# Performance work log

Measured on AMD Instinct MI355X. Metric: run time of the kernel, lower is better.

## Reference

```python
import jax, jax.numpy as jnp
import numpy as np

D_MODEL = 1024
NUM_HEADS = 16
HEAD_DIM = D_MODEL // NUM_HEADS
SCALE = HEAD_DIM ** -0.5


def setup_inputs() -> dict:
    key = jax.random.key(0)
    k1, k2, k3 = jax.random.split(key, 3)
    B, N = 2, 2048
    x = jax.random.normal(k1, (B, N, D_MODEL), dtype=jnp.float32)
    w_qkv = jax.random.normal(k2, (D_MODEL, 3 * D_MODEL), dtype=jnp.float32) * (D_MODEL ** -0.5)
    b_qkv = jnp.zeros((3 * D_MODEL,), dtype=jnp.float32)
    w_proj = jax.random.normal(k3, (D_MODEL, D_MODEL), dtype=jnp.float32) * (D_MODEL ** -0.5)
    b_proj = jnp.zeros((D_MODEL,), dtype=jnp.float32)
    return {"x": x, "w_qkv": w_qkv, "b_qkv": b_qkv, "w_proj": w_proj, "b_proj": b_proj}


def reference(x, w_qkv, b_qkv, w_proj, b_proj):
    B, N, C = x.shape
    H, Hd = NUM_HEADS, HEAD_DIM
    # fused QKV projection: [B,N,3C] -> [3,B,H,N,Hd]
    qkv = (x @ w_qkv + b_qkv).reshape(B, N, 3, H, Hd).transpose(2, 0, 3, 1, 4)
    q, k, v = qkv[0], qkv[1], qkv[2]
    # manual scaled dot-product attention (full NxN scores, as in source)
    attn = jnp.einsum('bhqd,bhkd->bhqk', q, k) * SCALE
    attn = jax.nn.softmax(attn, axis=-1)
    out = jnp.einsum('bhqk,bhkd->bhqd', attn, v)  # [B,H,N,Hd]
    out = out.transpose(0, 2, 1, 3).reshape(B, N, C)
    return out @ w_proj + b_proj
```

## Files before the change

kernel.cpp:

```cpp
#include <hip/hip_runtime.h>
#include <hip/hip_bf16.h>
#include <stdint.h>

typedef __attribute__((ext_vector_type(8))) __bf16 bf16x8;
typedef __attribute__((ext_vector_type(4))) __bf16 bf16x4;
typedef __attribute__((ext_vector_type(4))) float f32x4;

#define AS1 __attribute__((address_space(1)))
#define AS3 __attribute__((address_space(3)))

__device__ __forceinline__ void load_lds16(const void* g, void* l) {
    __builtin_amdgcn_global_load_lds((const AS1 void*)g, (AS3 void*)l, 16, 0, 0);
}

__device__ __forceinline__ float m3(float a, float b, float c) {
    return fmaxf(fmaxf(a, b), c);
}

constexpr float QSCALE = 0.18033688011112042f;

__device__ __forceinline__ int sigma32(int kv) {
    return (kv < 16) ? ((kv >> 2) * 8 + (kv & 3))
                     : (((kv - 16) >> 2) * 8 + 4 + ((kv - 16) & 3));
}

__global__ void cvt_x(const float4* __restrict__ x, bf16x4* __restrict__ o, int n4) {
    int i = blockIdx.x * blockDim.x + threadIdx.x;
    if (i >= n4) return;
    float4 v = x[i];
    bf16x4 r;
    r[0] = (__bf16)v.x; r[1] = (__bf16)v.y; r[2] = (__bf16)v.z; r[3] = (__bf16)v.w;
    o[i] = r;
}

__global__ void tconv(const float* __restrict__ src, __bf16* __restrict__ dst,
                      int R, int C) {
    __shared__ float tile[32][33];
    int c0 = blockIdx.x * 32, r0 = blockIdx.y * 32;
    int tx = threadIdx.x, ty = threadIdx.y;
    #pragma unroll
    for (int i = 0; i < 32; i += 8)
        tile[ty + i][tx] = src[(size_t)(r0 + ty + i) * C + c0 + tx];
    __syncthreads();
    #pragma unroll
    for (int i = 0; i < 32; i += 8)
        dst[(size_t)(c0 + ty + i) * R + r0 + tx] = (__bf16)tile[tx][ty + i];
}

template <int MODE>
__global__ __launch_bounds__(256)
void gemm128(const __bf16* __restrict__ A, const __bf16* __restrict__ Bt,
             const float* __restrict__ bias, void* __restrict__ outp,
             int M, int Nn, int K) {
    __shared__ __bf16 As[128][32];
    __shared__ __bf16 Bs[128][32];
    const int t = threadIdx.x;
    const int w = t >> 6, l = t & 63;
    const int lrow = l & 15, lhi = l >> 4;
    const int wr = (w >> 1) * 64, wc = (w & 1) * 64;
    const int m0 = blockIdx.y * 128, n0 = blockIdx.x * 128;

    f32x4 acc[4][4] = {};

    const int sr = t >> 2, sc = (t & 3) * 8;
    const __bf16* ag = A + (size_t)(m0 + sr) * K + sc;
    const __bf16* bg = Bt + (size_t)(n0 + sr) * K + sc;

    for (int kt = 0; kt < K; kt += 32) {
        load_lds16(ag, &As[sr][sc]);
        load_lds16(ag + (size_t)64 * K, &As[64 + sr][sc]);
        load_lds16(bg, &Bs[sr][sc]);
        load_lds16(bg + (size_t)64 * K, &Bs[64 + sr][sc]);
        ag += 32; bg += 32;
        __syncthreads();
        bf16x8 af[4], bfv[4];
        #pragma unroll
        for (int i = 0; i < 4; ++i)
            af[i] = *(const bf16x8*)(&As[wr + i * 16 + lrow][lhi * 8]);
        #pragma unroll
        for (int j = 0; j < 4; ++j)
            bfv[j] = *(const bf16x8*)(&Bs[wc + j * 16 + lrow][lhi * 8]);
        #pragma unroll
        for (int i = 0; i < 4; ++i)
            #pragma unroll
            for (int j = 0; j < 4; ++j)
                acc[i][j] = __builtin_amdgcn_mfma_f32_16x16x32_bf16(
                    af[i], bfv[j], acc[i][j], 0, 0, 0);
        __syncthreads();
    }

    #pragma unroll
    for (int i = 0; i < 4; ++i)
        #pragma unroll
        for (int j = 0; j < 4; ++j)
            #pragma unroll
            for (int r = 0; r < 4; ++r) {
                int row = m0 + wr + i * 16 + lhi * 4 + r;
                int col = n0 + wc + j * 16 + lrow;
                float val = acc[i][j][r] + bias[col];
                if (MODE == 0) {
                    int which = col >> 10;
                    int h = (col >> 6) & 15;
                    int d = col & 63;
                    int b = row >> 11;
                    int n = row & 2047;
                    int bh = (b << 4) + h;
                    if (which == 2) {
                        ((__bf16*)outp)[(size_t)2 * (32 * 2048 * 64) +
                                        ((size_t)bh * 64 + d) * 2048 +
                                        (n & ~31) + sigma32(n & 31)] = (__bf16)val;
                    } else {
                        if (which == 0) val *= QSCALE;
                        ((__bf16*)outp)[(size_t)which * (32 * 2048 * 64) +
                                        ((size_t)bh * 2048 + n) * 64 + d] = (__bf16)val;
                    }
                } else {
                    ((float*)outp)[(size_t)row * Nn + col] = val;
                }
            }
}

__global__ __launch_bounds__(256)
void attn_fwd(const __bf16* __restrict__ q, const __bf16* __restrict__ k,
              const __bf16* __restrict__ vt, __bf16* __restrict__ out) {
    __shared__ __bf16 KsV[2][64][64];
    __shared__ __bf16 VsV[2][64][64];
    char* ksB = (char*)KsV;
    char* vsB = (char*)VsV;

    const int t = threadIdx.x;
    const int w = t >> 6, l = t & 63;
    const int lrow = l & 15, lhi = l >> 4;
    const int bh = blockIdx.y;
    const int q0 = blockIdx.x * 128 + w * 32;

    const __bf16* qp = q + ((size_t)bh * 2048 + q0) * 64;
    bf16x8 qfA0 = *(const bf16x8*)(qp + lrow * 64 + lhi * 8);
    bf16x8 qfA1 = *(const bf16x8*)(qp + lrow * 64 + 32 + lhi * 8);
    bf16x8 qfB0 = *(const bf16x8*)(qp + (16 + lrow) * 64 + lhi * 8);
    bf16x8 qfB1 = *(const bf16x8*)(qp + (16 + lrow) * 64 + 32 + lhi * 8);

    f32x4 oA[4] = {}, oB[4] = {};
    float mA = -1e30f, mB = -1e30f;
    float lA = 0.f, lB = 0.f;

    const __bf16* kg = k + (size_t)bh * 2048 * 64;
    const __bf16* vg = vt + (size_t)bh * 64 * 2048;

    const int sr = t >> 3;
    const int sw8 = ((t & 7) ^ (sr & 7)) * 8;
    const int rsw = (lrow & 7) << 4;

    {
        char* kd = ksB + t * 16;
        char* vd = vsB + t * 16;
        load_lds16(kg + (size_t)sr * 64 + sw8, kd);
        load_lds16(kg + (size_t)(32 + sr) * 64 + sw8, kd + 4096);
        load_lds16(vg + (size_t)sr * 2048 + sw8, vd);
        load_lds16(vg + (size_t)(32 + sr) * 2048 + sw8, vd + 4096);
    }

    const __bf16* kst  = kg + (size_t)(64 + sr) * 64 + sw8;
    const __bf16* kst2 = kst + 32 * 64;
    const __bf16* vst  = vg + (size_t)sr * 2048 + 64 + sw8;
    const __bf16* vst2 = vst + 32 * 2048;

    int cur = 0;
    for (int kv0 = 0; kv0 < 2048; kv0 += 64) {
        __syncthreads();
        if (kv0 + 64 < 2048) {
            char* kd = ksB + (cur ^ 1) * 8192 + t * 16;
            char* vd = vsB + (cur ^ 1) * 8192 + t * 16;
            load_lds16(kst, kd);
            load_lds16(kst2, kd + 4096);
            load_lds16(vst, vd);
            load_lds16(vst2, vd + 4096);
            kst += 4096; kst2 += 4096; vst += 64; vst2 += 64;
        }
        const char* kb = ksB + cur * 8192 + lrow * 128;
        const char* vb = vsB + cur * 8192 + lrow * 128;
        const int o0 = (lhi << 4) ^ rsw;
        const int o4 = ((4 + lhi) << 4) ^ rsw;

        f32x4 sA0 = {}, sA1 = {}, sA2 = {}, sA3 = {};
        f32x4 sB0 = {}, sB1 = {}, sB2 = {}, sB3 = {};
        __builtin_amdgcn_s_setprio(1);
        {
            bf16x8 kf0, kf1;
#define QK_GROUP(SA, SB, BASE)                                                 \
            kf0 = *(const bf16x8*)(kb + (BASE) + o0);                          \
            kf1 = *(const bf16x8*)(kb + (BASE) + o4);                          \
            SA = __builtin_amdgcn_mfma_f32_16x16x32_bf16(kf0, qfA0, SA, 0, 0, 0); \
            SA = __builtin_amdgcn_mfma_f32_16x16x32_bf16(kf1, qfA1, SA, 0, 0, 0); \
            SB = __builtin_amdgcn_mfma_f32_16x16x32_bf16(kf0, qfB0, SB, 0, 0, 0); \
            SB = __builtin_amdgcn_mfma_f32_16x16x32_bf16(kf1, qfB1, SB, 0, 0, 0);
            QK_GROUP(sA0, sB0, 0)
            QK_GROUP(sA1, sB1, 2048)
            QK_GROUP(sA2, sB2, 4096)
            QK_GROUP(sA3, sB3, 6144)
#undef QK_GROUP
        }
        __builtin_amdgcn_s_setprio(0);

        float u0 = m3(sA0[0], sA0[1], sA0[2]);
        float u1 = m3(sA0[3], sA1[0], sA1[1]);
        float u2 = m3(sA1[2], sA1[3], sA2[0]);
        float u3 = m3(sA2[1], sA2[2], sA2[3]);
        float u4 = m3(sA3[0], sA3[1], sA3[2]);
        float tmA = fmaxf(m3(u0, u1, u2), m3(u3, u4, sA3[3]));
        float v0 = m3(sB0[0], sB0[1], sB0[2]);
        float v1 = m3(sB0[3], sB1[0], sB1[1]);
        float v2 = m3(sB1[2], sB1[3], sB2[0]);
        float v3 = m3(sB2[1], sB2[2], sB2[3]);
        float v4 = m3(sB3[0], sB3[1], sB3[2]);
        float tmB = fmaxf(m3(v0, v1, v2), m3(v3, v4, sB3[3]));
        tmA = fmaxf(tmA, __shfl_xor(tmA, 16, 64));
        tmA = fmaxf(tmA, __shfl_xor(tmA, 32, 64));
        tmB = fmaxf(tmB, __shfl_xor(tmB, 16, 64));
        tmB = fmaxf(tmB, __shfl_xor(tmB, 32, 64));
        if (!__all(tmA <= mA + 8.0f && tmB <= mB + 8.0f)) {
            float mnA = fmaxf(mA, tmA), mnB = fmaxf(mB, tmB);
            float cA = __builtin_amdgcn_exp2f(mA - mnA);
            float cB = __builtin_amdgcn_exp2f(mB - mnB);
            lA *= cA; lB *= cB;
            #pragma unroll
            for (int dt = 0; dt < 4; ++dt)
                #pragma unroll
                for (int r = 0; r < 4; ++r) { oA[dt][r] *= cA; oB[dt][r] *= cB; }
            mA = mnA; mB = mnB;
        }
        float pA[16], pB[16];
        #pragma unroll
        for (int r = 0; r < 4; ++r) {
            pA[r]      = __builtin_amdgcn_exp2f(sA0[r] - mA);
            pA[4 + r]  = __builtin_amdgcn_exp2f(sA1[r] - mA);
            pA[8 + r]  = __builtin_amdgcn_exp2f(sA2[r] - mA);
            pA[12 + r] = __builtin_amdgcn_exp2f(sA3[r] - mA);
            pB[r]      = __builtin_amdgcn_exp2f(sB0[r] - mB);
            pB[4 + r]  = __builtin_amdgcn_exp2f(sB1[r] - mB);
            pB[8 + r]  = __builtin_amdgcn_exp2f(sB2[r] - mB);
            pB[12 + r] = __builtin_amdgcn_exp2f(sB3[r] - mB);
        }
        float rsA = 0.f, rsB = 0.f;
        #pragma unroll
        for (int j = 0; j < 16; ++j) { rsA += pA[j]; rsB += pB[j]; }
        lA += rsA; lB += rsB;

        bf16x8 pfA0, pfA1, pfB0, pfB1;
        #pragma unroll
        for (int j = 0; j < 8; ++j) {
            pfA0[j] = (__bf16)pA[j]; pfA1[j] = (__bf16)pA[8 + j];
            pfB0[j] = (__bf16)pB[j]; pfB1[j] = (__bf16)pB[8 + j];
        }

        __builtin_amdgcn_s_setprio(1);
        #pragma unroll
        for (int dt = 0; dt < 4; ++dt) {
            bf16x8 vf0 = *(const bf16x8*)(vb + dt * 2048 + o0);
            bf16x8 vf1 = *(const bf16x8*)(vb + dt * 2048 + o4);
            oA[dt] = __builtin_amdgcn_mfma_f32_16x16x32_bf16(vf0, pfA0, oA[dt], 0, 0, 0);
            oA[dt] = __builtin_amdgcn_mfma_f32_16x16x32_bf16(vf1, pfA1, oA[dt], 0, 0, 0);
            oB[dt] = __builtin_amdgcn_mfma_f32_16x16x32_bf16(vf0, pfB0, oB[dt], 0, 0, 0);
            oB[dt] = __builtin_amdgcn_mfma_f32_16x16x32_bf16(vf1, pfB1, oB[dt], 0, 0, 0);
        }
        __builtin_amdgcn_s_setprio(0);
        cur ^= 1;
    }

    lA += __shfl_xor(lA, 16, 64); lA += __shfl_xor(lA, 32, 64);
    lB += __shfl_xor(lB, 16, 64); lB += __shfl_xor(lB, 32, 64);
    float invA = __builtin_amdgcn_rcpf(lA);
    float invB = __builtin_amdgcn_rcpf(lB);

    const int b = bh >> 4, h = bh & 15;
    __bf16* orowA = out + ((size_t)(b * 2048 + q0 + lrow)) * 1024 + h * 64;
    __bf16* orowB = out + ((size_t)(b * 2048 + q0 + 16 + lrow)) * 1024 + h * 64;
    #pragma unroll
    for (int dt = 0; dt < 4; ++dt) {
        bf16x4 ovA, ovB;
        #pragma unroll
        for (int r = 0; r < 4; ++r) {
            ovA[r] = (__bf16)(oA[dt][r] * invA);
            ovB[r] = (__bf16)(oB[dt][r] * invB);
        }
        *(bf16x4*)(orowA + dt * 16 + lhi * 4) = ovA;
        *(bf16x4*)(orowB + dt * 16 + lhi * 4) = ovB;
    }
}

extern "C" void kernel_launch(void* const* d_in, const int* in_sizes, int n_in,
                              void* d_out, int out_size, void* d_ws, size_t ws_size,
                              hipStream_t stream) {
    const float* x      = (const float*)d_in[0];
    const float* w_qkv  = (const float*)d_in[1];
    const float* b_qkv  = (const float*)d_in[2];
    const float* w_proj = (const float*)d_in[3];
    const float* b_proj = (const float*)d_in[4];
    float* out = (float*)d_out;

    __bf16* ws     = (__bf16*)d_ws;
    __bf16* x_bf   = ws;
    __bf16* wqkvT  = x_bf + 4096 * 1024;
    __bf16* wprojT = wqkvT + 3072 * 1024;
    __bf16* qb     = wprojT + 1024 * 1024;
    __bf16* kb     = qb + 32 * 2048 * 64;
    __bf16* vtb    = kb + 32 * 2048 * 64;
    __bf16* attn   = vtb + 32 * 2048 * 64;

    cvt_x<<<4096, 256, 0, stream>>>((const float4*)x, (bf16x4*)x_bf, 4096 * 1024 / 4);
    tconv<<<dim3(96, 32), dim3(32, 8), 0, stream>>>(w_qkv, wqkvT, 1024, 3072);
    tconv<<<dim3(32, 32), dim3(32, 8), 0, stream>>>(w_proj, wprojT, 1024, 1024);
    gemm128<0><<<dim3(24, 32), 256, 0, stream>>>(x_bf, wqkvT, b_qkv, qb, 4096, 3072, 1024);
    attn_fwd<<<dim3(16, 32), 256, 0, stream>>>(qb, kb, vtb, attn);
    gemm128<1><<<dim3(8, 32), 256, 0, stream>>>(attn, wprojT, b_proj, out, 4096, 1024, 1024);
}
```

Baseline: 218.1 us.

## Split attention over KV halves with a separate combine kernel

Adds a split-KV (flash-decoding style) attention path. Each of two z-slices processes half of the keys and writes unnormalized fp32 partial outputs plus running max and sum. A combine kernel then merges the two halves and writes bf16 output. This doubles the grid from 512 to 1024 blocks to improve occupancy and CU fill, at the cost of extra fp32 partial traffic and one more launch. The new path is used only when the workspace is large enough, otherwise the original kernel runs.

New measurement: 228.9 us. 1.05x slower.

```diff
diff --git a/kernel.cpp b/kernel.cpp
--- a/kernel.cpp
+++ b/kernel.cpp
@@ -288,6 +288,202 @@
     }
 }
 
+__global__ __launch_bounds__(256)
+void attn_part(const __bf16* __restrict__ q, const __bf16* __restrict__ k,
+               const __bf16* __restrict__ vt, float* __restrict__ opart,
+               float* __restrict__ ml) {
+    __shared__ __bf16 KsV[2][64][64];
+    __shared__ __bf16 VsV[2][64][64];
+    char* ksB = (char*)KsV;
+    char* vsB = (char*)VsV;
+
+    const int t = threadIdx.x;
+    const int w = t >> 6, l = t & 63;
+    const int lrow = l & 15, lhi = l >> 4;
+    const int bh = blockIdx.y;
+    const int z = blockIdx.z;
+    const int kvb = z * 1024;
+    const int q0 = blockIdx.x * 128 + w * 32;
+
+    const __bf16* qp = q + ((size_t)bh * 2048 + q0) * 64;
+    bf16x8 qfA0 = *(const bf16x8*)(qp + lrow * 64 + lhi * 8);
+    bf16x8 qfA1 = *(const bf16x8*)(qp + lrow * 64 + 32 + lhi * 8);
+    bf16x8 qfB0 = *(const bf16x8*)(qp + (16 + lrow) * 64 + lhi * 8);
+    bf16x8 qfB1 = *(const bf16x8*)(qp + (16 + lrow) * 64 + 32 + lhi * 8);
+
+    f32x4 oA[4] = {}, oB[4] = {};
+    float mA = -1e30f, mB = -1e30f;
+    float lA = 0.f, lB = 0.f;
+
+    const __bf16* kg = k + (size_t)bh * 2048 * 64;
+    const __bf16* vg = vt + (size_t)bh * 64 * 2048;
+
+    const int sr = t >> 3;
+    const int sw8 = ((t & 7) ^ (sr & 7)) * 8;
+    const int rsw = (lrow & 7) << 4;
+
+    {
+        char* kd = ksB + t * 16;
+        char* vd = vsB + t * 16;
+        load_lds16(kg + (size_t)(kvb + sr) * 64 + sw8, kd);
+        load_lds16(kg + (size_t)(kvb + 32 + sr) * 64 + sw8, kd + 4096);
+        load_lds16(vg + (size_t)sr * 2048 + kvb + sw8, vd);
+        load_lds16(vg + (size_t)(32 + sr) * 2048 + kvb + sw8, vd + 4096);
+    }
+
+    const __bf16* kst  = kg + (size_t)(kvb + 64 + sr) * 64 + sw8;
+    const __bf16* kst2 = kst + 32 * 64;
+    const __bf16* vst  = vg + (size_t)sr * 2048 + kvb + 64 + sw8;
+    const __bf16* vst2 = vst + 32 * 2048;
+
+    int cur = 0;
+    for (int step = 0; step < 16; ++step) {
+        __syncthreads();
+        if (step < 15) {
+            char* kd = ksB + (cur ^ 1) * 8192 + t * 16;
+            char* vd = vsB + (cur ^ 1) * 8192 + t * 16;
+            load_lds16(kst, kd);
+            load_lds16(kst2, kd + 4096);
+            load_lds16(vst, vd);
+            load_lds16(vst2, vd + 4096);
+            kst += 4096; kst2 += 4096; vst += 64; vst2 += 64;
+        }
+        const char* kb = ksB + cur * 8192 + lrow * 128;
+        const char* vb = vsB + cur * 8192 + lrow * 128;
+        const int o0 = (lhi << 4) ^ rsw;
+        const int o4 = ((4 + lhi) << 4) ^ rsw;
+
+        f32x4 sA0 = {}, sA1 = {}, sA2 = {}, sA3 = {};
+        f32x4 sB0 = {}, sB1 = {}, sB2 = {}, sB3 = {};
+        __builtin_amdgcn_s_setprio(1);
+        {
+            bf16x8 kf0, kf1;
+#define QK_GROUP(SA, SB, BASE)                                                 \
+            kf0 = *(const bf16x8*)(kb + (BASE) + o0);                          \
+            kf1 = *(const bf16x8*)(kb + (BASE) + o4);                          \
+            SA = __builtin_amdgcn_mfma_f32_16x16x32_bf16(kf0, qfA0, SA, 0, 0, 0); \
+            SA = __builtin_amdgcn_mfma_f32_16x16x32_bf16(kf1, qfA1, SA, 0, 0, 0); \
+            SB = __builtin_amdgcn_mfma_f32_16x16x32_bf16(kf0, qfB0, SB, 0, 0, 0); \
+            SB = __builtin_amdgcn_mfma_f32_16x16x32_bf16(kf1, qfB1, SB, 0, 0, 0);
+            QK_GROUP(sA0, sB0, 0)
+            QK_GROUP(sA1, sB1, 2048)
+            QK_GROUP(sA2, sB2, 4096)
+            QK_GROUP(sA3, sB3, 6144)
+#undef QK_GROUP
+        }
+        __builtin_amdgcn_s_setprio(0);
+
+        float u0 = m3(sA0[0], sA0[1], sA0[2]);
+        float u1 = m3(sA0[3], sA1[0], sA1[1]);
+        float u2 = m3(sA1[2], sA1[3], sA2[0]);
+        float u3 = m3(sA2[1], sA2[2], sA2[3]);
+        float u4 = m3(sA3[0], sA3[1], sA3[2]);
+        float tmA = fmaxf(m3(u0, u1, u2), m3(u3, u4, sA3[3]));
+        float v0 = m3(sB0[0], sB0[1], sB0[2]);
+        float v1 = m3(sB0[3], sB1[0], sB1[1]);
+        float v2 = m3(sB1[2], sB1[3], sB2[0]);
+        float v3 = m3(sB2[1], sB2[2], sB2[3]);
+        float v4 = m3(sB3[0], sB3[1], sB3[2]);
+        float tmB = fmaxf(m3(v0, v1, v2), m3(v3, v4, sB3[3]));
+        tmA = fmaxf(tmA, __shfl_xor(tmA, 16, 64));
+        tmA = fmaxf(tmA, __shfl_xor(tmA, 32, 64));
+        tmB = fmaxf(tmB, __shfl_xor(tmB, 16, 64));
+        tmB = fmaxf(tmB, __shfl_xor(tmB, 32, 64));
+        if (!__all(tmA <= mA + 8.0f && tmB <= mB + 8.0f)) {
+            float mnA = fmaxf(mA, tmA), mnB = fmaxf(mB, tmB);
+            float cA = __builtin_amdgcn_exp2f(mA - mnA);
+            float cB = __builtin_amdgcn_exp2f(mB - mnB);
+            lA *= cA; lB *= cB;
+            #pragma unroll
+            for (int dt = 0; dt < 4; ++dt)
+                #pragma unroll
+                for (int r = 0; r < 4; ++r) { oA[dt][r] *= cA; oB[dt][r] *= cB; }
+            mA = mnA; mB = mnB;
+        }
+        float pA[16], pB[16];
+        #pragma unroll
+        for (int r = 0; r < 4; ++r) {
+            pA[r]      = __builtin_amdgcn_exp2f(sA0[r] - mA);
+            pA[4 + r]  = __builtin_amdgcn_exp2f(sA1[r] - mA);
+            pA[8 + r]  = __builtin_amdgcn_exp2f(sA2[r] - mA);
+            pA[12 + r] = __builtin_amdgcn_exp2f(sA3[r] - mA);
+            pB[r]      = __builtin_amdgcn_exp2f(sB0[r] - mB);
+            pB[4 + r]  = __builtin_amdgcn_exp2f(sB1[r] - mB);
+            pB[8 + r]  = __builtin_amdgcn_exp2f(sB2[r] - mB);
+            pB[12 + r] = __builtin_amdgcn_exp2f(sB3[r] - mB);
+        }
+        float rsA = 0.f, rsB = 0.f;
+        #pragma unroll
+        for (int j = 0; j < 16; ++j) { rsA += pA[j]; rsB += pB[j]; }
+        lA += rsA; lB += rsB;
+
+        bf16x8 pfA0, pfA1, pfB0, pfB1;
+        #pragma unroll
+        for (int j = 0; j < 8; ++j) {
+            pfA0[j] = (__bf16)pA[j]; pfA1[j] = (__bf16)pA[8 + j];
+            pfB0[j] = (__bf16)pB[j]; pfB1[j] = (__bf16)pB[8 + j];
+        }
+
+        __builtin_amdgcn_s_setprio(1);
+        #pragma unroll
+        for (int dt = 0; dt < 4; ++dt) {
+            bf16x8 vf0 = *(const bf16x8*)(vb + dt * 2048 + o0);
+            bf16x8 vf1 = *(const bf16x8*)(vb + dt * 2048 + o4);
+            oA[dt] = __builtin_amdgcn_mfma_f32_16x16x32_bf16(vf0, pfA0, oA[dt], 0, 0, 0);
+            oA[dt] = __builtin_amdgcn_mfma_f32_16x16x32_bf16(vf1, pfA1, oA[dt], 0, 0, 0);
+            oB[dt] = __builtin_amdgcn_mfma_f32_16x16x32_bf16(vf0, pfB0, oB[dt], 0, 0, 0);
+            oB[dt] = __builtin_amdgcn_mfma_f32_16x16x32_bf16(vf1, pfB1, oB[dt], 0, 0, 0);
+        }
+        __builtin_amdgcn_s_setprio(0);
+        cur ^= 1;
+    }
+
+    lA += __shfl_xor(lA, 16, 64); lA += __shfl_xor(lA, 32, 64);
+    lB += __shfl_xor(lB, 16, 64); lB += __shfl_xor(lB, 32, 64);
+
+    const size_t zoff = (size_t)z * (32 * 2048 * 64);
+    float* opA = opart + zoff + ((size_t)bh * 2048 + q0 + lrow) * 64;
+    float* opB = opart + zoff + ((size_t)bh * 2048 + q0 + 16 + lrow) * 64;
+    #pragma unroll
+    for (int dt = 0; dt < 4; ++dt) {
+        *(f32x4*)(opA + dt * 16 + lhi * 4) = oA[dt];
+        *(f32x4*)(opB + dt * 16 + lhi * 4) = oB[dt];
+    }
+    if (lhi == 0) {
+        float* mlA = ml + ((size_t)z * (32 * 2048) + (size_t)bh * 2048 + q0 + lrow) * 2;
+        float* mlB = ml + ((size_t)z * (32 * 2048) + (size_t)bh * 2048 + q0 + 16 + lrow) * 2;
+        mlA[0] = mA; mlA[1] = lA;
+        mlB[0] = mB; mlB[1] = lB;
+    }
+}
+
+__global__ __launch_bounds__(256)
+void attn_combine(const float* __restrict__ opart, const float* __restrict__ ml,
+                  __bf16* __restrict__ out) {
+    const int idx = blockIdx.x * 256 + threadIdx.x;
+    const int d4 = idx & 15;
+    const int qrow = (idx >> 4) & 2047;
+    const int bh = idx >> 15;
+
+    const size_t row = (size_t)bh * 2048 + qrow;
+    const float2 ml0 = *(const float2*)(ml + row * 2);
+    const float2 ml1 = *(const float2*)(ml + ((size_t)(32 * 2048) + row) * 2);
+    const f32x4 o0 = *(const f32x4*)(opart + row * 64 + d4 * 4);
+    const f32x4 o1 = *(const f32x4*)(opart + (size_t)(32 * 2048 * 64) + row * 64 + d4 * 4);
+
+    float M = fmaxf(ml0.x, ml1.x);
+    float w0 = __builtin_amdgcn_exp2f(ml0.x - M);
+    float w1 = __builtin_amdgcn_exp2f(ml1.x - M);
+    float inv = __builtin_amdgcn_rcpf(ml0.y * w0 + ml1.y * w1);
+
+    const int b = bh >> 4, h = bh & 15;
+    bf16x4 ov;
+    #pragma unroll
+    for (int r = 0; r < 4; ++r)
+        ov[r] = (__bf16)((o0[r] * w0 + o1[r] * w1) * inv);
+    *(bf16x4*)(out + ((size_t)(b * 2048 + qrow)) * 1024 + h * 64 + d4 * 4) = ov;
+}
+
 extern "C" void kernel_launch(void* const* d_in, const int* in_sizes, int n_in,
                               void* d_out, int out_size, void* d_ws, size_t ws_size,
                               hipStream_t stream) {
@@ -306,11 +502,24 @@
     __bf16* kb     = qb + 32 * 2048 * 64;
     __bf16* vtb    = kb + 32 * 2048 * 64;
     __bf16* attn   = vtb + 32 * 2048 * 64;
+    float*  opart  = (float*)(attn + 4096 * 1024);
+    float*  mlbuf  = opart + 2 * 32 * 2048 * 64;
+
+    const size_t need = (size_t)(mlbuf + 2 * 32 * 2048 * 2 - (float*)d_ws) * 4 / 1;
+    const size_t need_bytes = ((char*)(mlbuf + 2 * 32 * 2048 * 2)) - ((char*)d_ws);
+    (void)need;
 
     cvt_x<<<4096, 256, 0, stream>>>((const float4*)x, (bf16x4*)x_bf, 4096 * 1024 / 4);
     tconv<<<dim3(96, 32), dim3(32, 8), 0, stream>>>(w_qkv, wqkvT, 1024, 3072);
     tconv<<<dim3(32, 32), dim3(32, 8), 0, stream>>>(w_proj, wprojT, 1024, 1024);
     gemm128<0><<<dim3(24, 32), 256, 0, stream>>>(x_bf, wqkvT, b_qkv, qb, 4096, 3072, 1024);
-    attn_fwd<<<dim3(16, 32), 256, 0, stream>>>(qb, kb, vtb, attn);
+
+    if (ws_size >= need_bytes) {
+        attn_part<<<dim3(16, 32, 2), 256, 0, stream>>>(qb, kb, vtb, opart, mlbuf);
+        attn_combine<<<4096, 256, 0, stream>>>(opart, mlbuf, attn);
+    } else {
+        attn_fwd<<<dim3(16, 32), 256, 0, stream>>>(qb, kb, vtb, attn);
+    }
+
     gemm128<1><<<dim3(8, 32), 256, 0, stream>>>(attn, wprojT, b_proj, out, 4096, 1024, 1024);
 }
```

## Triple-buffer GEMM LDS loads with swizzle, XCD block remap, and MFMA priority

Applied to the files above, without the earlier changes.

Rewrites the gemm128 main loop as a three-stage pipeline that prefetches K-tiles two steps ahead through async global-to-LDS loads, controlled by explicit vmcnt waits and raw barriers. It also XOR-swizzles the LDS column layout to cut bank conflicts, remaps the flat block index so neighbouring tiles are spread across XCDs, and raises wave priority around the MFMA block. The goal is to hide global load latency and LDS conflicts, at the cost of three times the LDS footprint and fragile hand-written wait counts.

Result: faster. 208.5 us (-4.4%).

```diff
diff --git a/kernel.cpp b/kernel.cpp
--- a/kernel.cpp
+++ b/kernel.cpp
@@ -52,42 +52,77 @@
 void gemm128(const __bf16* __restrict__ A, const __bf16* __restrict__ Bt,
              const float* __restrict__ bias, void* __restrict__ outp,
              int M, int Nn, int K) {
-    __shared__ __bf16 As[128][32];
-    __shared__ __bf16 Bs[128][32];
+    __shared__ __bf16 As[3][128][32];
+    __shared__ __bf16 Bs[3][128][32];
     const int t = threadIdx.x;
     const int w = t >> 6, l = t & 63;
     const int lrow = l & 15, lhi = l >> 4;
     const int wr = (w >> 1) * 64, wc = (w & 1) * 64;
-    const int m0 = blockIdx.y * 128, n0 = blockIdx.x * 128;
+
+    int nwg = gridDim.x * gridDim.y;
+    int flat = blockIdx.x + blockIdx.y * gridDim.x;
+    if ((nwg & 7) == 0) flat = (flat & 7) * (nwg >> 3) + (flat >> 3);
+    const int m0 = (flat / gridDim.x) * 128;
+    const int n0 = (flat % gridDim.x) * 128;
 
     f32x4 acc[4][4] = {};
 
-    const int sr = t >> 2, sc = (t & 3) * 8;
-    const __bf16* ag = A + (size_t)(m0 + sr) * K + sc;
-    const __bf16* bg = Bt + (size_t)(n0 + sr) * K + sc;
-
-    for (int kt = 0; kt < K; kt += 32) {
-        load_lds16(ag, &As[sr][sc]);
-        load_lds16(ag + (size_t)64 * K, &As[64 + sr][sc]);
-        load_lds16(bg, &Bs[sr][sc]);
-        load_lds16(bg + (size_t)64 * K, &Bs[64 + sr][sc]);
-        ag += 32; bg += 32;
-        __syncthreads();
+    const int sr = t >> 2;
+    const int dc = (t & 3) * 8;
+    const int scsw = ((t & 3) ^ ((sr >> 1) & 3)) * 8;
+    const __bf16* agb = A + (size_t)(m0 + sr) * K + scsw;
+    const __bf16* bgb = Bt + (size_t)(n0 + sr) * K + scsw;
+
+#define STAGE_G(BUF, KT)                                                   \
+    { load_lds16(agb + (KT), &As[BUF][sr][dc]);                            \
+      load_lds16(agb + (size_t)64 * K + (KT), &As[BUF][64 + sr][dc]);      \
+      load_lds16(bgb + (KT), &Bs[BUF][sr][dc]);                            \
+      load_lds16(bgb + (size_t)64 * K + (KT), &Bs[BUF][64 + sr][dc]); }
+
+    STAGE_G(0, 0)
+    STAGE_G(1, 32)
+
+    const int rofs = (lhi ^ ((lrow >> 1) & 3)) << 4;
+    const int nt = K >> 5;
+    int cur = 0, pre = 2;
+    for (int tt = 0; tt < nt; ++tt) {
+        if (tt + 2 < nt) {
+            STAGE_G(pre, (tt + 2) * 32)
+            asm volatile("s_waitcnt vmcnt(8)" ::: "memory");
+        } else if (tt + 1 < nt) {
+            asm volatile("s_waitcnt vmcnt(4)" ::: "memory");
+        } else {
+            asm volatile("s_waitcnt vmcnt(0)" ::: "memory");
+        }
+        __builtin_amdgcn_sched_barrier(0);
+        __builtin_amdgcn_s_barrier();
+        __builtin_amdgcn_sched_barrier(0);
+
         bf16x8 af[4], bfv[4];
         #pragma unroll
         for (int i = 0; i < 4; ++i)
-            af[i] = *(const bf16x8*)(&As[wr + i * 16 + lrow][lhi * 8]);
+            af[i] = *(const bf16x8*)((const char*)&As[cur][wr + i * 16 + lrow][0] + rofs);
         #pragma unroll
         for (int j = 0; j < 4; ++j)
-            bfv[j] = *(const bf16x8*)(&Bs[wc + j * 16 + lrow][lhi * 8]);
+            bfv[j] = *(const bf16x8*)((const char*)&Bs[cur][wc + j * 16 + lrow][0] + rofs);
+        __builtin_amdgcn_s_setprio(1);
         #pragma unroll
         for (int i = 0; i < 4; ++i)
             #pragma unroll
             for (int j = 0; j < 4; ++j)
                 acc[i][j] = __builtin_amdgcn_mfma_f32_16x16x32_bf16(
                     af[i], bfv[j], acc[i][j], 0, 0, 0);
-        __syncthreads();
+        __builtin_amdgcn_s_setprio(0);
+
+        __builtin_amdgcn_sched_barrier(0);
+        asm volatile("s_waitcnt lgkmcnt(0)" ::: "memory");
+        __builtin_amdgcn_s_barrier();
+        __builtin_amdgcn_sched_barrier(0);
+
+        cur = (cur == 2) ? 0 : cur + 1;
+        pre = (pre == 2) ? 0 : pre + 1;
     }
+#undef STAGE_G
 
     #pragma unroll
     for (int i = 0; i < 4; ++i)
```
